# Kernel optimization log

Measured on AMD Instinct MI355X. Metric: run time of the kernel, lower is better.

Reference implementation:

```python
import jax, jax.numpy as jnp
import numpy as np

N = 50000   # nodes
E = 640000  # edges
IN, H, OUT = 128, 128, 64
BN_EPS = 1e-5


def setup_inputs() -> dict:
    key = jax.random.key(0)
    ks = jax.random.split(key, 16)
    inp = {}
    inp["x"] = jax.random.normal(ks[0], (N, IN), jnp.float32)
    inp["edge_index"] = jax.random.randint(ks[1], (2, E), 0, N, dtype=jnp.int32)
    # BatchNorm affine params (nontrivial so grads are informative)
    inp["bn_in_gamma"] = 1.0 + 0.1 * jax.random.normal(ks[2], (IN,), jnp.float32)
    inp["bn_in_beta"] = 0.1 * jax.random.normal(ks[3], (IN,), jnp.float32)
    inp["bn1_gamma"] = 1.0 + 0.1 * jax.random.normal(ks[4], (H,), jnp.float32)
    inp["bn1_beta"] = 0.1 * jax.random.normal(ks[5], (H,), jnp.float32)
    inp["bn2_gamma"] = 1.0 + 0.1 * jax.random.normal(ks[6], (OUT,), jnp.float32)
    inp["bn2_beta"] = 0.1 * jax.random.normal(ks[7], (OUT,), jnp.float32)
    # Linear / GCNConv weights (fan-in scaled)
    inp["proj_W"] = jax.random.normal(ks[8], (IN, H), jnp.float32) / np.sqrt(IN)
    inp["proj_b"] = jnp.zeros((H,), jnp.float32)
    inp["conv1_W"] = jax.random.normal(ks[9], (H, H), jnp.float32) / np.sqrt(H)
    inp["conv1_b"] = jnp.zeros((H,), jnp.float32)
    inp["conv2_W"] = jax.random.normal(ks[10], (H, OUT), jnp.float32) / np.sqrt(H)
    inp["conv2_b"] = jnp.zeros((OUT,), jnp.float32)
    return inp


def batchnorm(x, gamma, beta):
    # training-mode BN: batch statistics (biased variance), per-feature affine
    m = jnp.mean(x, axis=0)
    v = jnp.mean(jnp.square(x - m), axis=0)
    return (x - m) * jax.lax.rsqrt(v + BN_EPS) * gamma + beta


def gcn_conv(x, src, dst, W, b):
    # PyG GCNConv: y = D^{-1/2} (A + I) D^{-1/2} (x W) + b
    xw = x @ W                                    # [N, F_out]
    loops = jnp.arange(N, dtype=src.dtype)
    s = jnp.concatenate([src, loops])             # [E + N]
    d = jnp.concatenate([dst, loops])
    deg = jax.ops.segment_sum(jnp.ones_like(d, jnp.float32), d, num_segments=N)
    dinv = jnp.where(deg > 0, jax.lax.rsqrt(deg), 0.0)
    norm = dinv[s] * dinv[d]                      # [E + N]
    msgs = xw[s] * norm[:, None]                  # gather + per-edge scale
    out = jax.ops.segment_sum(msgs, d, num_segments=N)  # scatter-add
    return out + b


def reference(x, edge_index, bn_in_gamma, bn_in_beta, bn1_gamma, bn1_beta,
              bn2_gamma, bn2_beta, proj_W, proj_b, conv1_W, conv1_b,
              conv2_W, conv2_b):
    src, dst = edge_index[0], edge_index[1]
    h = batchnorm(x, bn_in_gamma, bn_in_beta)
    h = jax.nn.relu(h @ proj_W + proj_b)
    h = jax.nn.relu(batchnorm(gcn_conv(h, src, dst, conv1_W, conv1_b),
                              bn1_gamma, bn1_beta))
    # dropout: identity in eval mode
    out = batchnorm(gcn_conv(h, src, dst, conv2_W, conv2_b),
                    bn2_gamma, bn2_beta)
    return out
```

## Files before the change

kernel.cpp:

```cpp
#include <hip/hip_runtime.h>

#define NN 50000
#define NE 640000
#define BNEPS 1e-5f
#define NBANK 16
#define NBANKG 64
#define CAP 64

#define OFF_CURSOR 51200
#define OFF_ESRC 102400
#define OFF_WT0 1702400
#define OFF_WT1 1710592
#define OFF_WT2 1718784
#define OFF_STATS 1726976
#define OFF_B0 1755648
#define OFF_B1 8155648

typedef __attribute__((ext_vector_type(8))) __bf16 bf16x8;
typedef __attribute__((ext_vector_type(4))) float f32x4;

__device__ __forceinline__ float uplo(unsigned int u) {
  unsigned int v = u << 16;
  return __builtin_bit_cast(float, v);
}
__device__ __forceinline__ float uphi(unsigned int u) {
  unsigned int v = u & 0xffff0000u;
  return __builtin_bit_cast(float, v);
}
__device__ __forceinline__ unsigned int f2bf(float f) {
  unsigned int u = __builtin_bit_cast(unsigned int, f);
  return (u + 0x7fffu + ((u >> 16) & 1u)) >> 16;
}

__global__ __launch_bounds__(256) void prep_k(
    const float* __restrict__ W0, const float* __restrict__ W1,
    const float* __restrict__ W2, unsigned short* __restrict__ T0,
    unsigned short* __restrict__ T1, unsigned short* __restrict__ T2,
    int* __restrict__ cursor, float* __restrict__ stats) {
  const int bid = blockIdx.x;
  const int tid = threadIdx.x;
  if (bid < 160) {
    int f = bid * 256 + tid;
    if (f < 16384) {
      int k = f >> 7, n = f & 127;
      T0[n * 128 + k] = (unsigned short)f2bf(W0[f]);
    } else if (f < 32768) {
      int g = f - 16384;
      int k = g >> 7, n = g & 127;
      T1[n * 128 + k] = (unsigned short)f2bf(W1[g]);
    } else if (f < 40960) {
      int g = f - 32768;
      int k = g >> 6, n = g & 63;
      T2[n * 128 + k] = (unsigned short)f2bf(W2[g]);
    }
  } else if (bid < 356) {
    int i = (bid - 160) * 256 + tid;
    if (i < NN) cursor[i] = i * CAP;
  } else {
    int j = (bid - 356) * 256 + tid;
    stats[j] = 0.0f;
  }
}

template <int NC>
__device__ __forceinline__ void bn_stats_body(
    int sbid, int nsb, int tid, const float* __restrict__ A,
    float* __restrict__ sums, float* __restrict__ sqs, float (*rs)[NC],
    float (*rq)[NC]) {
  constexpr int CG = NC / 4;
  constexpr int RG = 256 / CG;
  const int tc = tid % CG;
  const int tr = tid / CG;
  float s0 = 0, s1 = 0, s2 = 0, s3 = 0, q0 = 0, q1 = 0, q2 = 0, q3 = 0;
  const int stride = nsb * RG;
  for (int r = sbid * RG + tr; r < NN; r += stride) {
    float4 v = *(const float4*)&A[(size_t)r * NC + tc * 4];
    s0 += v.x; s1 += v.y; s2 += v.z; s3 += v.w;
    q0 += v.x * v.x; q1 += v.y * v.y; q2 += v.z * v.z; q3 += v.w * v.w;
  }
  rs[tr][tc * 4] = s0; rs[tr][tc * 4 + 1] = s1;
  rs[tr][tc * 4 + 2] = s2; rs[tr][tc * 4 + 3] = s3;
  rq[tr][tc * 4] = q0; rq[tr][tc * 4 + 1] = q1;
  rq[tr][tc * 4 + 2] = q2; rq[tr][tc * 4 + 3] = q3;
  __syncthreads();
  if (tr == 0) {
    const int bank = (sbid & (NBANK - 1)) * NC;
    for (int j = 0; j < 4; ++j) {
      int c = tc * 4 + j;
      float ts = 0, tq = 0;
      for (int g = 0; g < RG; ++g) { ts += rs[g][c]; tq += rq[g][c]; }
      atomicAdd(&sums[bank + c], ts);
      atomicAdd(&sqs[bank + c], tq);
    }
  }
}

__global__ __launch_bounds__(256) void stats_fill_k(
    const float* __restrict__ x, float* __restrict__ s0,
    float* __restrict__ q0, const int* __restrict__ src,
    const int* __restrict__ dst, int* __restrict__ cursor,
    unsigned short* __restrict__ esrc) {
  __shared__ float rs[8][128];
  __shared__ float rq[8][128];
  const int bid = blockIdx.x;
  if (bid < 1024) {
    bn_stats_body<128>(bid, 1024, threadIdx.x, x, s0, q0, rs, rq);
  } else {
    int e = (bid - 1024) * 256 + threadIdx.x;
    if (e < NE / 2) {
      int p = atomicAdd(&cursor[dst[e]], 1);
      esrc[p] = (unsigned short)src[e];
    }
  }
}

__global__ __launch_bounds__(256) void fused12_fill_k(
    const float* __restrict__ x, const unsigned short* __restrict__ Wt0,
    const unsigned short* __restrict__ Wt1, const float* __restrict__ proj_b,
    const float* __restrict__ s0, const float* __restrict__ q0,
    const float* __restrict__ g0, const float* __restrict__ b0,
    unsigned short* __restrict__ Ybf, const int* __restrict__ src,
    const int* __restrict__ dst, int* __restrict__ cursor,
    unsigned short* __restrict__ esrc) {
  __shared__ __align__(16) char smem[17408];
  __shared__ float af_s[128];
  __shared__ float bf_s[128];
  __shared__ float pb_s[128];
  const int bid = blockIdx.x;
  const int tid = threadIdx.x;
  if (bid >= 782) {
    int e = NE / 2 + (bid - 782) * 256 + tid;
    if (e < NE) {
      int p = atomicAdd(&cursor[dst[e]], 1);
      esrc[p] = (unsigned short)src[e];
    }
    return;
  }
  const int row0 = bid * 64;
  if (tid < 128) {
    float s = 0.f, q = 0.f;
#pragma unroll
    for (int b = 0; b < NBANK; ++b) {
      s += s0[b * 128 + tid];
      q += q0[b * 128 + tid];
    }
    float m = s * (1.0f / NN);
    float v = q * (1.0f / NN) - m * m;
    float a = g0[tid] * rsqrtf(v + BNEPS);
    af_s[tid] = a;
    bf_s[tid] = b0[tid] - m * a;
    pb_s[tid] = proj_b[tid];
  }
  __syncthreads();
  for (int f = tid; f < 64 * 32; f += 256) {
    const int r = f >> 5;
    const int c4 = f & 31;
    const int rg = row0 + r;
    float4 v = make_float4(0.f, 0.f, 0.f, 0.f);
    if (rg < NN) {
      v = *(const float4*)&x[(size_t)rg * 128 + c4 * 4];
      const float4 a4 = *(const float4*)&af_s[c4 * 4];
      const float4 b4 = *(const float4*)&bf_s[c4 * 4];
      v.x = fmaf(a4.x, v.x, b4.x);
      v.y = fmaf(a4.y, v.y, b4.y);
      v.z = fmaf(a4.z, v.z, b4.z);
      v.w = fmaf(a4.w, v.w, b4.w);
    }
    uint2 wv;
    wv.x = f2bf(v.x) | (f2bf(v.y) << 16);
    wv.y = f2bf(v.z) | (f2bf(v.w) << 16);
    const int ba = (r * 256 + c4 * 8) ^ ((r & 7) << 4);
    *(uint2*)(smem + ba) = wv;
  }
  __syncthreads();

  const int w = tid >> 6;
  const int l = tid & 63;
  const int lr = l & 15;
  const int lg = l >> 4;
  const int arow = w * 16 + lr;
  f32x4 acc[8];
#pragma unroll
  for (int i = 0; i < 8; ++i) acc[i] = (f32x4){0.f, 0.f, 0.f, 0.f};
#pragma unroll
  for (int kt = 0; kt < 4; ++kt) {
    const int ba = (arow * 256 + kt * 64 + lg * 16) ^ ((arow & 7) << 4);
    bf16x8 a = __builtin_bit_cast(bf16x8, *(const uint4*)(smem + ba));
#pragma unroll
    for (int nt = 0; nt < 8; ++nt) {
      bf16x8 b = __builtin_bit_cast(
          bf16x8,
          *(const uint4*)&Wt0[(size_t)(nt * 16 + lr) * 128 + kt * 32 + lg * 8]);
      acc[nt] = __builtin_amdgcn_mfma_f32_16x16x32_bf16(a, b, acc[nt], 0, 0, 0);
    }
  }
  __syncthreads();
#pragma unroll
  for (int nt = 0; nt < 8; ++nt) {
    const float pb = pb_s[nt * 16 + lr];
#pragma unroll
    for (int r = 0; r < 4; ++r) {
      const int row = w * 16 + lg * 4 + r;
      const float hv = fmaxf(acc[nt][r] + pb, 0.f);
      const int ba = (row * 256 + (nt * 16 + lr) * 2) ^ ((row & 7) << 4);
      *(unsigned short*)(smem + ba) = (unsigned short)f2bf(hv);
    }
  }
  __syncthreads();
  f32x4 acc2[8];
#pragma unroll
  for (int i = 0; i < 8; ++i) acc2[i] = (f32x4){0.f, 0.f, 0.f, 0.f};
#pragma unroll
  for (int kt = 0; kt < 4; ++kt) {
    const int ba = (arow * 256 + kt * 64 + lg * 16) ^ ((arow & 7) << 4);
    bf16x8 a = __builtin_bit_cast(bf16x8, *(const uint4*)(smem + ba));
#pragma unroll
    for (int nt = 0; nt < 8; ++nt) {
      bf16x8 b = __builtin_bit_cast(
          bf16x8,
          *(const uint4*)&Wt1[(size_t)(nt * 16 + lr) * 128 + kt * 32 + lg * 8]);
      acc2[nt] =
          __builtin_amdgcn_mfma_f32_16x16x32_bf16(a, b, acc2[nt], 0, 0, 0);
    }
  }
  float* Cl = (float*)smem;
  const int tcx = tid % 32;
  const int trx = tid / 32;
#pragma unroll
  for (int half = 0; half < 2; ++half) {
    __syncthreads();
    if ((w >> 1) == half) {
#pragma unroll
      for (int nt = 0; nt < 8; ++nt)
#pragma unroll
        for (int r = 0; r < 4; ++r)
          Cl[((w & 1) * 16 + lg * 4 + r) * 132 + nt * 16 + lr] = acc2[nt][r];
    }
    __syncthreads();
#pragma unroll
    for (int i = 0; i < 4; ++i) {
      const int rl = trx * 4 + i;
      const int rg = row0 + half * 32 + rl;
      if (rg < NN) {
        float4 v = *(const float4*)&Cl[rl * 132 + tcx * 4];
        uint2 o;
        o.x = f2bf(v.x) | (f2bf(v.y) << 16);
        o.y = f2bf(v.z) | (f2bf(v.w) << 16);
        *(uint2*)&Ybf[(size_t)rg * 128 + tcx * 4] = o;
      }
    }
  }
}

template <int NC, int OUTBF>
__global__ __launch_bounds__(256) void gather_bf_k(
    const int* __restrict__ cursor, const unsigned short* __restrict__ esrc,
    const unsigned short* __restrict__ Y, void* __restrict__ outp,
    const float* __restrict__ cb, float* __restrict__ sums,
    float* __restrict__ sqs) {
  constexpr int CG = NC / 8;
  constexpr int RG = 256 / CG;
  __shared__ float ws_s[4][NC];
  __shared__ float ws_q[4][NC];
  const int tid = threadIdx.x;
  const int tc = tid % CG;
  const int tr = tid / CG;
  const int n = blockIdx.x * RG + tr;
  const bool act = (n < NN);
  const int c = tc * 8;
  float z[8];
#pragma unroll
  for (int j = 0; j < 8; ++j) z[j] = 0.f;
  if (act) {
    const int beg = n * CAP;
    const int end = cursor[n];
    const float dn = rsqrtf((float)(end - beg) + 1.0f);
    float a[8];
    {
      const uint4 p = *(const uint4*)&Y[(size_t)n * NC + c];
      a[0] = dn * uplo(p.x); a[1] = dn * uphi(p.x);
      a[2] = dn * uplo(p.y); a[3] = dn * uphi(p.y);
      a[4] = dn * uplo(p.z); a[5] = dn * uphi(p.z);
      a[6] = dn * uplo(p.w); a[7] = dn * uphi(p.w);
    }
    int e = beg;
    for (; e + 2 <= end; e += 2) {
      const int s0 = esrc[e];
      const int s1 = esrc[e + 1];
      const float d0 = rsqrtf((float)(cursor[s0] - s0 * CAP) + 1.0f);
      const float d1 = rsqrtf((float)(cursor[s1] - s1 * CAP) + 1.0f);
      const uint4 q0 = *(const uint4*)&Y[(size_t)s0 * NC + c];
      const uint4 q1 = *(const uint4*)&Y[(size_t)s1 * NC + c];
      a[0] = fmaf(d0, uplo(q0.x), a[0]); a[1] = fmaf(d0, uphi(q0.x), a[1]);
      a[2] = fmaf(d0, uplo(q0.y), a[2]); a[3] = fmaf(d0, uphi(q0.y), a[3]);
      a[4] = fmaf(d0, uplo(q0.z), a[4]); a[5] = fmaf(d0, uphi(q0.z), a[5]);
      a[6] = fmaf(d0, uplo(q0.w), a[6]); a[7] = fmaf(d0, uphi(q0.w), a[7]);
      a[0] = fmaf(d1, uplo(q1.x), a[0]); a[1] = fmaf(d1, uphi(q1.x), a[1]);
      a[2] = fmaf(d1, uplo(q1.y), a[2]); a[3] = fmaf(d1, uphi(q1.y), a[3]);
      a[4] = fmaf(d1, uplo(q1.z), a[4]); a[5] = fmaf(d1, uphi(q1.z), a[5]);
      a[6] = fmaf(d1, uplo(q1.w), a[6]); a[7] = fmaf(d1, uphi(q1.w), a[7]);
    }
    if (e < end) {
      const int s0 = esrc[e];
      const float d0 = rsqrtf((float)(cursor[s0] - s0 * CAP) + 1.0f);
      const uint4 q0 = *(const uint4*)&Y[(size_t)s0 * NC + c];
      a[0] = fmaf(d0, uplo(q0.x), a[0]); a[1] = fmaf(d0, uphi(q0.x), a[1]);
      a[2] = fmaf(d0, uplo(q0.y), a[2]); a[3] = fmaf(d0, uphi(q0.y), a[3]);
      a[4] = fmaf(d0, uplo(q0.z), a[4]); a[5] = fmaf(d0, uphi(q0.z), a[5]);
      a[6] = fmaf(d0, uplo(q0.w), a[6]); a[7] = fmaf(d0, uphi(q0.w), a[7]);
    }
#pragma unroll
    for (int j = 0; j < 8; ++j) z[j] = fmaf(dn, a[j], cb[c + j]);
    if constexpr (OUTBF == 1) {
      unsigned int p[4];
#pragma unroll
      for (int j = 0; j < 4; ++j)
        p[j] = f2bf(z[2 * j]) | (f2bf(z[2 * j + 1]) << 16);
      *(uint4*)&((unsigned short*)outp)[(size_t)n * NC + c] =
          make_uint4(p[0], p[1], p[2], p[3]);
    } else {
      float* Z = (float*)outp;
      *(float4*)&Z[(size_t)n * NC + c] = make_float4(z[0], z[1], z[2], z[3]);
      *(float4*)&Z[(size_t)n * NC + c + 4] =
          make_float4(z[4], z[5], z[6], z[7]);
    }
  }
  float s[8], q[8];
#pragma unroll
  for (int j = 0; j < 8; ++j) { s[j] = z[j]; q[j] = z[j] * z[j]; }
#pragma unroll
  for (int off = CG; off < 64; off <<= 1) {
#pragma unroll
    for (int j = 0; j < 8; ++j) {
      s[j] += __shfl_xor(s[j], off);
      q[j] += __shfl_xor(q[j], off);
    }
  }
  const int w = tid >> 6;
  const int l = tid & 63;
  if (l < CG) {
    *(float4*)&ws_s[w][c] = make_float4(s[0], s[1], s[2], s[3]);
    *(float4*)&ws_s[w][c + 4] = make_float4(s[4], s[5], s[6], s[7]);
    *(float4*)&ws_q[w][c] = make_float4(q[0], q[1], q[2], q[3]);
    *(float4*)&ws_q[w][c + 4] = make_float4(q[4], q[5], q[6], q[7]);
  }
  __syncthreads();
  if (tid < NC) {
    float ts = 0.f, tq = 0.f;
#pragma unroll
    for (int g = 0; g < 4; ++g) { ts += ws_s[g][tid]; tq += ws_q[g][tid]; }
    const int bank = (blockIdx.x % NBANKG) * NC;
    atomicAdd(&sums[bank + tid], ts);
    atomicAdd(&sqs[bank + tid], tq);
  }
}

__global__ __launch_bounds__(256) void conv2_k(
    const unsigned short* __restrict__ Z1, const unsigned short* __restrict__ Wt,
    const float* __restrict__ sums, const float* __restrict__ sqs,
    const float* __restrict__ gamma, const float* __restrict__ beta,
    unsigned short* __restrict__ O1) {
  __shared__ __align__(16) char smem[16384];
  __shared__ float af_s[128];
  __shared__ float bf_s[128];
  const int tid = threadIdx.x;
  const int row0 = blockIdx.x * 64;
  if (tid < 128) {
    float s = 0.f, q = 0.f;
#pragma unroll
    for (int b = 0; b < NBANKG; ++b) {
      s += sums[b * 128 + tid];
      q += sqs[b * 128 + tid];
    }
    float m = s * (1.0f / NN);
    float v = q * (1.0f / NN) - m * m;
    float a = gamma[tid] * rsqrtf(v + BNEPS);
    af_s[tid] = a;
    bf_s[tid] = beta[tid] - m * a;
  }
  __syncthreads();
  for (int f = tid; f < 64 * 16; f += 256) {
    const int r = f >> 4;
    const int c8 = f & 15;
    const int rg = row0 + r;
    uint4 w4 = make_uint4(0u, 0u, 0u, 0u);
    if (rg < NN) {
      const uint4 raw = *(const uint4*)&Z1[(size_t)rg * 128 + c8 * 8];
      const int cc = c8 * 8;
      float e[8] = {uplo(raw.x), uphi(raw.x), uplo(raw.y), uphi(raw.y),
                    uplo(raw.z), uphi(raw.z), uplo(raw.w), uphi(raw.w)};
      unsigned int p[4];
#pragma unroll
      for (int j = 0; j < 4; ++j) {
        float lo = fmaxf(fmaf(af_s[cc + 2 * j], e[2 * j], bf_s[cc + 2 * j]), 0.f);
        float hi = fmaxf(
            fmaf(af_s[cc + 2 * j + 1], e[2 * j + 1], bf_s[cc + 2 * j + 1]), 0.f);
        p[j] = f2bf(lo) | (f2bf(hi) << 16);
      }
      w4 = make_uint4(p[0], p[1], p[2], p[3]);
    }
    const int ba = (r * 256 + c8 * 16) ^ ((r & 7) << 4);
    *(uint4*)(smem + ba) = w4;
  }
  __syncthreads();
  const int w = tid >> 6;
  const int l = tid & 63;
  const int lr = l & 15;
  const int lg = l >> 4;
  const int arow = w * 16 + lr;
  f32x4 acc[4];
#pragma unroll
  for (int i = 0; i < 4; ++i) acc[i] = (f32x4){0.f, 0.f, 0.f, 0.f};
#pragma unroll
  for (int kt = 0; kt < 4; ++kt) {
    const int ba = (arow * 256 + kt * 64 + lg * 16) ^ ((arow & 7) << 4);
    bf16x8 a = __builtin_bit_cast(bf16x8, *(const uint4*)(smem + ba));
#pragma unroll
    for (int nt = 0; nt < 4; ++nt) {
      bf16x8 b = __builtin_bit_cast(
          bf16x8,
          *(const uint4*)&Wt[(size_t)(nt * 16 + lr) * 128 + kt * 32 + lg * 8]);
      acc[nt] = __builtin_amdgcn_mfma_f32_16x16x32_bf16(a, b, acc[nt], 0, 0, 0);
    }
  }
  float* Cl = (float*)smem;
  const int tcx = tid % 16;
  const int trx = tid / 16;
#pragma unroll
  for (int half = 0; half < 2; ++half) {
    __syncthreads();
    if ((w >> 1) == half) {
#pragma unroll
      for (int nt = 0; nt < 4; ++nt)
#pragma unroll
        for (int r = 0; r < 4; ++r)
          Cl[((w & 1) * 16 + lg * 4 + r) * 68 + nt * 16 + lr] = acc[nt][r];
    }
    __syncthreads();
#pragma unroll
    for (int i = 0; i < 2; ++i) {
      const int rl = trx * 2 + i;
      const int rg = row0 + half * 32 + rl;
      if (rg < NN) {
        float4 v = *(const float4*)&Cl[rl * 68 + tcx * 4];
        uint2 o;
        o.x = f2bf(v.x) | (f2bf(v.y) << 16);
        o.y = f2bf(v.z) | (f2bf(v.w) << 16);
        *(uint2*)&O1[(size_t)rg * 64 + tcx * 4] = o;
      }
    }
  }
}

__global__ __launch_bounds__(256) void final_k(
    const float* __restrict__ Z2, const float* __restrict__ s2,
    const float* __restrict__ q2, const float* __restrict__ gamma,
    const float* __restrict__ beta, float* __restrict__ out) {
  __shared__ float af_s[64];
  __shared__ float bf_s[64];
  if (threadIdx.x < 64) {
    float s = 0.f, q = 0.f;
#pragma unroll
    for (int b = 0; b < NBANKG; ++b) {
      s += s2[b * 64 + threadIdx.x];
      q += q2[b * 64 + threadIdx.x];
    }
    float m = s * (1.0f / NN);
    float v = q * (1.0f / NN) - m * m;
    float a = gamma[threadIdx.x] * rsqrtf(v + BNEPS);
    af_s[threadIdx.x] = a;
    bf_s[threadIdx.x] = beta[threadIdx.x] - m * a;
  }
  __syncthreads();
  const int u = blockIdx.x * 256 + threadIdx.x;
  if (u >= NN * 16) return;
  const int r = u >> 4;
  const int c = (u & 15) * 4;
  float4 v = *(const float4*)&Z2[(size_t)r * 64 + c];
  const float4 a4 = *(const float4*)&af_s[c];
  const float4 b4 = *(const float4*)&bf_s[c];
  float4 o;
  o.x = fmaf(a4.x, v.x, b4.x);
  o.y = fmaf(a4.y, v.y, b4.y);
  o.z = fmaf(a4.z, v.z, b4.z);
  o.w = fmaf(a4.w, v.w, b4.w);
  *(float4*)&out[(size_t)r * 64 + c] = o;
}

extern "C" void kernel_launch(void* const* d_in, const int* in_sizes, int n_in,
                              void* d_out, int out_size, void* d_ws,
                              size_t ws_size, hipStream_t stream) {
  const float* x = (const float*)d_in[0];
  const int* ei = (const int*)d_in[1];
  const int* src = ei;
  const int* dst = ei + NE;
  const float* bn_in_g = (const float*)d_in[2];
  const float* bn_in_b = (const float*)d_in[3];
  const float* bn1_g = (const float*)d_in[4];
  const float* bn1_b = (const float*)d_in[5];
  const float* bn2_g = (const float*)d_in[6];
  const float* bn2_b = (const float*)d_in[7];
  const float* proj_W = (const float*)d_in[8];
  const float* proj_b = (const float*)d_in[9];
  const float* conv1_W = (const float*)d_in[10];
  const float* conv1_b = (const float*)d_in[11];
  const float* conv2_W = (const float*)d_in[12];
  const float* conv2_b = (const float*)d_in[13];
  float* out = (float*)d_out;

  float* ws = (float*)d_ws;
  int* cursor = (int*)(ws + OFF_CURSOR);
  unsigned short* esrc = (unsigned short*)(ws + OFF_ESRC);
  unsigned short* Wt0 = (unsigned short*)(ws + OFF_WT0);
  unsigned short* Wt1 = (unsigned short*)(ws + OFF_WT1);
  unsigned short* Wt2 = (unsigned short*)(ws + OFF_WT2);
  float* st = ws + OFF_STATS;
  float* s0 = st;
  float* q0 = st + 2048;
  float* s1 = st + 4096;
  float* q1 = st + 12288;
  float* s2 = st + 20480;
  float* q2 = st + 24576;
  float* B0 = ws + OFF_B0;
  float* B1 = ws + OFF_B1;
  unsigned short* Ybf = (unsigned short*)B1;
  unsigned short* Z1bf = (unsigned short*)B0;
  unsigned short* Y2bf = (unsigned short*)B1;
  float* Z2 = B0;

  prep_k<<<468, 256, 0, stream>>>(proj_W, conv1_W, conv2_W, Wt0, Wt1, Wt2,
                                  cursor, st);
  stats_fill_k<<<2274, 256, 0, stream>>>(x, s0, q0, src, dst, cursor, esrc);
  fused12_fill_k<<<2032, 256, 0, stream>>>(x, Wt0, Wt1, proj_b, s0, q0,
                                           bn_in_g, bn_in_b, Ybf, src, dst,
                                           cursor, esrc);
  gather_bf_k<128, 1><<<3125, 256, 0, stream>>>(cursor, esrc, Ybf, Z1bf,
                                                conv1_b, s1, q1);
  conv2_k<<<782, 256, 0, stream>>>(Z1bf, Wt2, s1, q1, bn1_g, bn1_b, Y2bf);
  gather_bf_k<64, 0><<<1563, 256, 0, stream>>>(cursor, esrc, Y2bf, Z2, conv2_b,
                                               s2, q2);
  final_k<<<(NN * 16 + 255) / 256, 256, 0, stream>>>(Z2, s2, q2, bn2_g, bn2_b,
                                                     out);
}
```

Baseline: 150.3 us.

## Replace direct CSR edge fill with two-pass bucketed destination sort

Edge insertion into per-node slots becomes two passes. First, all edges are binned into 256 coarse destination buckets, packed as (dst<<16|src). Then one block per bucket scatters its edges into the per-node CAP slots, so the atomics and esrc writes stay within a small address window for better locality. This adds an extra pass over the edges plus a bucket buffer, and it clamps bucket and node capacities. Edges are silently dropped if a bucket holds more than BCAP or a node more than CAP.

```diff
diff --git a/kernel.cpp b/kernel.cpp
--- a/kernel.cpp
+++ b/kernel.cpp
@@ -6,6 +6,9 @@
 #define NBANK 16
 #define NBANKG 64
 #define CAP 64
+#define NBUCK 256
+#define BUCKW 196
+#define BCAP 3008
 
 #define OFF_CURSOR 51200
 #define OFF_ESRC 102400
@@ -13,8 +16,10 @@
 #define OFF_WT1 1710592
 #define OFF_WT2 1718784
 #define OFF_STATS 1726976
-#define OFF_B0 1755648
-#define OFF_B1 8155648
+#define OFF_BCUR 1755648
+#define OFF_EBUF 1755904
+#define OFF_B0 2525952
+#define OFF_B1 8925952
 
 typedef __attribute__((ext_vector_type(8))) __bf16 bf16x8;
 typedef __attribute__((ext_vector_type(4))) float f32x4;
@@ -36,7 +41,8 @@
     const float* __restrict__ W0, const float* __restrict__ W1,
     const float* __restrict__ W2, unsigned short* __restrict__ T0,
     unsigned short* __restrict__ T1, unsigned short* __restrict__ T2,
-    int* __restrict__ cursor, float* __restrict__ stats) {
+    int* __restrict__ cursor, float* __restrict__ stats,
+    int* __restrict__ bcur) {
   const int bid = blockIdx.x;
   const int tid = threadIdx.x;
   if (bid < 160) {
@@ -56,9 +62,11 @@
   } else if (bid < 356) {
     int i = (bid - 160) * 256 + tid;
     if (i < NN) cursor[i] = i * CAP;
-  } else {
+  } else if (bid < 468) {
     int j = (bid - 356) * 256 + tid;
     stats[j] = 0.0f;
+  } else {
+    if (tid < NBUCK) bcur[tid] = 0;
   }
 }
 
@@ -95,11 +103,11 @@
   }
 }
 
-__global__ __launch_bounds__(256) void stats_fill_k(
+__global__ __launch_bounds__(256) void stats_bucketA_k(
     const float* __restrict__ x, float* __restrict__ s0,
     float* __restrict__ q0, const int* __restrict__ src,
-    const int* __restrict__ dst, int* __restrict__ cursor,
-    unsigned short* __restrict__ esrc) {
+    const int* __restrict__ dst, int* __restrict__ bcur,
+    unsigned int* __restrict__ ebuf) {
   __shared__ float rs[8][128];
   __shared__ float rq[8][128];
   const int bid = blockIdx.x;
@@ -107,20 +115,23 @@
     bn_stats_body<128>(bid, 1024, threadIdx.x, x, s0, q0, rs, rq);
   } else {
     int e = (bid - 1024) * 256 + threadIdx.x;
-    if (e < NE / 2) {
-      int p = atomicAdd(&cursor[dst[e]], 1);
-      esrc[p] = (unsigned short)src[e];
-    }
-  }
-}
-
-__global__ __launch_bounds__(256) void fused12_fill_k(
+    if (e < NE) {
+      const int d = dst[e];
+      const int b = d / BUCKW;
+      const int p = atomicAdd(&bcur[b], 1);
+      if (p < BCAP)
+        ebuf[b * BCAP + p] = ((unsigned int)d << 16) | (unsigned int)src[e];
+    }
+  }
+}
+
+__global__ __launch_bounds__(256) void fused12_bucketB_k(
     const float* __restrict__ x, const unsigned short* __restrict__ Wt0,
     const unsigned short* __restrict__ Wt1, const float* __restrict__ proj_b,
     const float* __restrict__ s0, const float* __restrict__ q0,
     const float* __restrict__ g0, const float* __restrict__ b0,
-    unsigned short* __restrict__ Ybf, const int* __restrict__ src,
-    const int* __restrict__ dst, int* __restrict__ cursor,
+    unsigned short* __restrict__ Ybf, const int* __restrict__ bcur,
+    const unsigned int* __restrict__ ebuf, int* __restrict__ cursor,
     unsigned short* __restrict__ esrc) {
   __shared__ __align__(16) char smem[17408];
   __shared__ float af_s[128];
@@ -129,10 +140,17 @@
   const int bid = blockIdx.x;
   const int tid = threadIdx.x;
   if (bid >= 782) {
-    int e = NE / 2 + (bid - 782) * 256 + tid;
-    if (e < NE) {
-      int p = atomicAdd(&cursor[dst[e]], 1);
-      esrc[p] = (unsigned short)src[e];
+    const int b = bid - 782;
+    int nb = bcur[b];
+    if (nb > BCAP) nb = BCAP;
+    const unsigned int* eb = &ebuf[b * BCAP];
+    for (int i = tid; i < nb; i += 256) {
+      const unsigned int u = eb[i];
+      const int d = (int)(u >> 16);
+      const int s = (int)(u & 0xffffu);
+      const int p = atomicAdd(&cursor[d], 1);
+      if (p < (d + 1) * CAP)
+        esrc[p] = (unsigned short)s;
     }
     return;
   }
@@ -273,7 +291,8 @@
   for (int j = 0; j < 8; ++j) z[j] = 0.f;
   if (act) {
     const int beg = n * CAP;
-    const int end = cursor[n];
+    int end = cursor[n];
+    if (end > beg + CAP) end = beg + CAP;
     const float dn = rsqrtf((float)(end - beg) + 1.0f);
     float a[8];
     {
@@ -521,6 +540,8 @@
   float* q1 = st + 12288;
   float* s2 = st + 20480;
   float* q2 = st + 24576;
+  int* bcur = (int*)(ws + OFF_BCUR);
+  unsigned int* ebuf = (unsigned int*)(ws + OFF_EBUF);
   float* B0 = ws + OFF_B0;
   float* B1 = ws + OFF_B1;
   unsigned short* Ybf = (unsigned short*)B1;
@@ -528,12 +549,12 @@
   unsigned short* Y2bf = (unsigned short*)B1;
   float* Z2 = B0;
 
-  prep_k<<<468, 256, 0, stream>>>(proj_W, conv1_W, conv2_W, Wt0, Wt1, Wt2,
-                                  cursor, st);
-  stats_fill_k<<<2274, 256, 0, stream>>>(x, s0, q0, src, dst, cursor, esrc);
-  fused12_fill_k<<<2032, 256, 0, stream>>>(x, Wt0, Wt1, proj_b, s0, q0,
-                                           bn_in_g, bn_in_b, Ybf, src, dst,
-                                           cursor, esrc);
+  prep_k<<<469, 256, 0, stream>>>(proj_W, conv1_W, conv2_W, Wt0, Wt1, Wt2,
+                                  cursor, st, bcur);
+  stats_bucketA_k<<<3524, 256, 0, stream>>>(x, s0, q0, src, dst, bcur, ebuf);
+  fused12_bucketB_k<<<1038, 256, 0, stream>>>(x, Wt0, Wt1, proj_b, s0, q0,
+                                              bn_in_g, bn_in_b, Ybf, bcur,
+                                              ebuf, cursor, esrc);
   gather_bf_k<128, 1><<<3125, 256, 0, stream>>>(cursor, esrc, Ybf, Z1bf,
                                                 conv1_b, s1, q1);
   conv2_k<<<782, 256, 0, stream>>>(Z1bf, Wt2, s1, q1, bn1_g, bn1_b, Y2bf);
```

After: 416.8 us. 2.77x slower.
